# Kernel optimization log

Hardware: AMD Instinct MI355X
Metric: run time of the kernel (lower is better)

The kernel has to match this reference:

```python
import jax, jax.numpy as jnp
import numpy as np

NF, EF, H, G, T, LAYERS = 133, 14, 300, 200, 12, 3
B, N_PER, PAIRS = 4096, 32, 32
N, E = B * N_PER, B * PAIRS * 2
R1, R2 = 550, 378  # readout dims per config defaults


def setup_inputs() -> dict:
    key = jax.random.key(0)
    ks = jax.random.split(key, 16)
    rng = np.random.default_rng(0)
    # edges within each graph, laid out as reverse pairs: 2i = (u->w), 2i+1 = (w->u)
    u = rng.integers(0, N_PER, size=(B, PAIRS))
    w = (u + 1 + rng.integers(0, N_PER - 1, size=(B, PAIRS))) % N_PER  # w != u
    offs = (np.arange(B) * N_PER)[:, None]
    u, w = u + offs, w + offs
    src = np.stack([u, w], axis=-1).reshape(-1).astype(np.int64)
    dst = np.stack([w, u], axis=-1).reshape(-1).astype(np.int64)
    node_graph = np.repeat(np.arange(B), N_PER).astype(np.int64)

    def lin(k, fin, fout):
        s = (2.0 / (fin + fout)) ** 0.5  # xavier_normal, gain=1
        return jax.random.normal(k, (fin, fout), jnp.float32) * s

    return {
        "v": jax.random.normal(ks[0], (N, NF + 1), jnp.float32),
        "e": jax.random.normal(ks[1], (E, EF + 1), jnp.float32),
        "globals_": jax.random.normal(ks[2], (B, G), jnp.float32),
        "Wi": lin(ks[3], NF + EF, H), "bi": jnp.zeros((H,), jnp.float32),
        "Wm": lin(ks[4], H, H), "bm": jnp.zeros((H,), jnp.float32),
        "Wa": lin(ks[5], NF + H, H), "ba": jnp.zeros((H,), jnp.float32),
        "Wr1": lin(ks[6], G + H, R1), "br1": jnp.zeros((R1,), jnp.float32),
        "Wr2": lin(ks[7], R1, R2), "br2": jnp.zeros((R2,), jnp.float32),
        "Wr3": lin(ks[8], R2, T), "br3": jnp.zeros((T,), jnp.float32),
        "src": jnp.asarray(src), "dst": jnp.asarray(dst),
        "node_graph": jnp.asarray(node_graph),
    }


def reference(v, e, globals_, Wi, bi, Wm, bm, Wa, ba,
              Wr1, br1, Wr2, br2, Wr3, br3, src, dst, node_graph):
    n = v.shape[0]
    b = globals_.shape[0]
    vv = v[:, :NF]          # strip trailing 'r' column
    ee = e[:, :EF]
    # edge init: h_0 = relu(W_i [src_v ; e])
    h0 = jax.nn.relu(jnp.concatenate([vv[src], ee], axis=1) @ Wi + bi)  # [E,H]
    rev = jnp.arange(h0.shape[0]) ^ 1  # reverse-pair edge layout
    h = h0
    for _ in range(LAYERS):
        # non-backtracking line-graph sum: incoming-to-src minus reverse edge
        acc = jax.ops.segment_sum(h, dst, num_segments=n)   # [N,H]
        m_e = acc[src] - h[rev]                             # [E,H]
        h = jax.nn.relu(h0 + m_e @ Wm + bm)                 # dropout p=0
    # reverse-graph copy_e sum => aggregate edges by ORIGINAL src node
    m_v = jax.ops.segment_sum(h, src, num_segments=n)       # [N,H]
    h_v = jax.nn.relu(jnp.concatenate([vv, m_v], axis=1) @ Wa + ba)
    # mean readout per graph
    cnt = jax.ops.segment_sum(jnp.ones((n,), v.dtype), node_graph, num_segments=b)
    out = jax.ops.segment_sum(h_v, node_graph, num_segments=b) / cnt[:, None]
    out = jax.nn.relu(jnp.concatenate([out, globals_], axis=1) @ Wr1 + br1)
    out = jax.nn.relu(out @ Wr2 + br2)
    return out @ Wr3 + br3
```

## Files before the change

### kernel.cpp

```cpp
#include <hip/hip_runtime.h>

typedef __bf16 bf16x8 __attribute__((ext_vector_type(8)));
typedef float f32x4 __attribute__((ext_vector_type(4)));
typedef unsigned short u16;
typedef unsigned int u32;
typedef unsigned long long u64;

#define NF_ 133
#define EF_ 14
#define HD 300
#define KH 320
#define K0 160
#define K2 448
#define NT 19

__device__ __forceinline__ u16 f2bf(float f) {
    union { float f; u32 u; } v; v.f = f;
    u32 r = v.u + 0x7fffu + ((v.u >> 16) & 1u);
    return (u16)(r >> 16);
}

__global__ void prep_w(const float* __restrict__ W, u16* __restrict__ Wt,
                       int K, int N, int KP, int NP) {
    int idx = blockIdx.x * 256 + threadIdx.x;
    if (idx >= NP * KP) return;
    int n = idx / KP, k = idx - n * KP;
    float val = (k < K && n < N) ? W[k * N + n] : 0.f;
    Wt[idx] = f2bf(val);
}

__global__ void prep_glob(const float* __restrict__ glob, u16* __restrict__ Ar1) {
    int idx = blockIdx.x * 256 + threadIdx.x;
    if (idx >= 4096 * 212) return;
    int g = idx / 212, c = 300 + (idx - g * 212);
    float val = (c < 500) ? glob[g * 200 + (c - 300)] : 0.f;
    Ar1[g * 512 + c] = f2bf(val);
}

__global__ __launch_bounds__(512, 1) void gnn_mega(
    const float* __restrict__ vf, const float* __restrict__ ef,
    const int* __restrict__ src, const int* __restrict__ dst,
    const u16* __restrict__ WiT, const u16* __restrict__ WmT, const u16* __restrict__ WaT,
    const float* __restrict__ bi, const float* __restrict__ bm, const float* __restrict__ ba,
    u16* __restrict__ Ar1)
{
    __shared__ u16 sm[64 * KH];
    __shared__ u16 shT[8 * 2560];
    __shared__ u16 sAe[8 * 512];
    __shared__ u16 sSo[8 * 256];
    __shared__ int s_src[64], s_dst[64];

    const int g = blockIdx.x;
    const int tid = threadIdx.x;
    const int wave = tid >> 6;
    const int lane = tid & 63;
    const int lm = lane & 15;
    const int q = lane >> 4;

    if (tid < 64) {
        s_src[tid] = src[g * 64 + tid] - g * 32;
        s_dst[tid] = dst[g * 64 + tid] - g * 32;
    }
    __syncthreads();

    for (int i = tid; i < 10240; i += 512) ((u32*)shT)[i] = 0u;
    if (tid < 512) ((u32*)sm)[9728 + tid] = 0u;

    for (int idx = tid; idx < 4096; idx += 512) {
        int e = idx >> 6, k = idx & 63;
        u16 v = (s_dst[k] == s_src[e] && k != (e ^ 1)) ? (u16)0x3F80 : (u16)0;
        sAe[((k >> 3) << 9) + (e << 3) + (k & 7)] = v;
    }
    for (int idx = tid; idx < 2048; idx += 512) {
        int n = idx >> 6, k = idx & 63;
        sSo[((k >> 3) << 8) + (n << 3) + (k & 7)] = (s_src[k] == n) ? (u16)0x3F80 : (u16)0;
    }
    for (int idx = tid; idx < 64 * K0; idx += 512) {
        int ed = idx / K0, c = idx - ed * K0;
        float val = 0.f;
        if (c < NF_) val = vf[(size_t)(g * 32 + s_src[ed]) * (NF_ + 1) + c];
        else if (c < NF_ + EF_) val = ef[(size_t)(g * 64 + ed) * (EF_ + 1) + (c - NF_)];
        sm[((c >> 3) << 9) + (ed << 3) + (c & 7)] = f2bf(val);
    }
    __syncthreads();

    f32x4 h0r[3][4];
    float bmv[3];
    {
        f32x4 acc[3][4];
        #pragma unroll
        for (int t = 0; t < 3; ++t)
            #pragma unroll
            for (int mt = 0; mt < 4; ++mt) acc[t][mt] = (f32x4){0.f, 0.f, 0.f, 0.f};
        #pragma unroll
        for (int ks = 0; ks < 5; ++ks) {
            bf16x8 af[4];
            #pragma unroll
            for (int mt = 0; mt < 4; ++mt)
                af[mt] = *(const bf16x8*)&sm[((ks * 4 + q) << 9) + ((mt * 16 + lm) << 3)];
            #pragma unroll
            for (int t = 0; t < 3; ++t) {
                int j = 8 * t + wave;
                if (j < NT) {
                    bf16x8 bfr = *(const bf16x8*)&WiT[(j * 16 + lm) * K0 + ks * 32 + q * 8];
                    #pragma unroll
                    for (int mt = 0; mt < 4; ++mt)
                        acc[t][mt] = __builtin_amdgcn_mfma_f32_16x16x32_bf16(af[mt], bfr, acc[t][mt], 0, 0, 0);
                }
            }
        }
        #pragma unroll
        for (int t = 0; t < 3; ++t) {
            int j = 8 * t + wave;
            int n = j * 16 + lm;
            bool ok = (j < NT) && (n < HD);
            float bv = ok ? bi[n] : 0.f;
            bmv[t] = ok ? bm[n] : 0.f;
            #pragma unroll
            for (int mt = 0; mt < 4; ++mt) {
                u64 w = 0;
                #pragma unroll
                for (int r = 0; r < 4; ++r) {
                    float hv = acc[t][mt][r] + bv;
                    hv = hv > 0.f ? hv : 0.f;
                    h0r[t][mt][r] = hv;
                    w |= ((u64)f2bf(hv)) << (16 * r);
                }
                if (ok) *(u64*)&shT[(mt * 2 + (q >> 1)) * 2560 + n * 8 + (q & 1) * 4] = w;
            }
        }
    }

    for (int layer = 0; layer < 3; ++layer) {
        __syncthreads();
        {
            bf16x8 ae[2][4];
            #pragma unroll
            for (int ks = 0; ks < 2; ++ks)
                #pragma unroll
                for (int mt = 0; mt < 4; ++mt)
                    ae[ks][mt] = *(const bf16x8*)&sAe[((ks * 4 + q) << 9) + ((mt * 16 + lm) << 3)];
            #pragma unroll
            for (int t = 0; t < 3; ++t) {
                int j = 8 * t + wave;
                if (j < NT) {
                    int col = j * 16 + lm;
                    f32x4 mac[4];
                    #pragma unroll
                    for (int mt = 0; mt < 4; ++mt) mac[mt] = (f32x4){0.f, 0.f, 0.f, 0.f};
                    #pragma unroll
                    for (int ks = 0; ks < 2; ++ks) {
                        bf16x8 bfr = *(const bf16x8*)&shT[(ks * 4 + q) * 2560 + col * 8];
                        #pragma unroll
                        for (int mt = 0; mt < 4; ++mt)
                            mac[mt] = __builtin_amdgcn_mfma_f32_16x16x32_bf16(ae[ks][mt], bfr, mac[mt], 0, 0, 0);
                    }
                    int base = ((col >> 3) << 9) + (col & 7);
                    #pragma unroll
                    for (int mt = 0; mt < 4; ++mt)
                        #pragma unroll
                        for (int r = 0; r < 4; ++r)
                            sm[base + ((mt * 16 + q * 4 + r) << 3)] = f2bf(mac[mt][r]);
                }
            }
        }
        __syncthreads();
        {
            f32x4 acc[3][4];
            #pragma unroll
            for (int t = 0; t < 3; ++t)
                #pragma unroll
                for (int mt = 0; mt < 4; ++mt) acc[t][mt] = (f32x4){0.f, 0.f, 0.f, 0.f};
            #pragma unroll
            for (int ks = 0; ks < 10; ++ks) {
                bf16x8 af[4];
                #pragma unroll
                for (int mt = 0; mt < 4; ++mt)
                    af[mt] = *(const bf16x8*)&sm[((ks * 4 + q) << 9) + ((mt * 16 + lm) << 3)];
                #pragma unroll
                for (int t = 0; t < 3; ++t) {
                    int j = 8 * t + wave;
                    if (j < NT) {
                        bf16x8 bfr = *(const bf16x8*)&WmT[(j * 16 + lm) * KH + ks * 32 + q * 8];
                        #pragma unroll
                        for (int mt = 0; mt < 4; ++mt)
                            acc[t][mt] = __builtin_amdgcn_mfma_f32_16x16x32_bf16(af[mt], bfr, acc[t][mt], 0, 0, 0);
                    }
                }
            }
            #pragma unroll
            for (int t = 0; t < 3; ++t) {
                int j = 8 * t + wave;
                int n = j * 16 + lm;
                bool ok = (j < NT) && (n < HD);
                #pragma unroll
                for (int mt = 0; mt < 4; ++mt) {
                    u64 w = 0;
                    #pragma unroll
                    for (int r = 0; r < 4; ++r) {
                        float hv = h0r[t][mt][r] + acc[t][mt][r] + bmv[t];
                        hv = hv > 0.f ? hv : 0.f;
                        w |= ((u64)f2bf(hv)) << (16 * r);
                    }
                    if (ok) *(u64*)&shT[(mt * 2 + (q >> 1)) * 2560 + n * 8 + (q & 1) * 4] = w;
                }
            }
        }
    }
    __syncthreads();

    for (int idx = tid; idx < 32 * K2; idx += 512) {
        int n = idx / K2, c = idx - n * K2;
        float val = (c < NF_) ? vf[(size_t)(g * 32 + n) * (NF_ + 1) + c] : 0.f;
        sm[((c >> 3) << 8) + (n << 3) + (c & 7)] = f2bf(val);
    }
    __syncthreads();

    #pragma unroll
    for (int t = 0; t < 3; ++t) {
        int j = 8 * t + wave;
        if (j < NT) {
            int hc = j * 16 + lm;
            f32x4 vacc[2];
            #pragma unroll
            for (int mt = 0; mt < 2; ++mt) vacc[mt] = (f32x4){0.f, 0.f, 0.f, 0.f};
            #pragma unroll
            for (int ks = 0; ks < 2; ++ks) {
                bf16x8 bfr = *(const bf16x8*)&shT[(ks * 4 + q) * 2560 + hc * 8];
                #pragma unroll
                for (int mt = 0; mt < 2; ++mt) {
                    bf16x8 af = *(const bf16x8*)&sSo[((ks * 4 + q) << 8) + ((mt * 16 + lm) << 3)];
                    vacc[mt] = __builtin_amdgcn_mfma_f32_16x16x32_bf16(af, bfr, vacc[mt], 0, 0, 0);
                }
            }
            if (hc < HD) {
                int cc = NF_ + hc;
                int base = ((cc >> 3) << 8) + (cc & 7);
                #pragma unroll
                for (int mt = 0; mt < 2; ++mt)
                    #pragma unroll
                    for (int r = 0; r < 4; ++r)
                        sm[base + ((mt * 16 + q * 4 + r) << 3)] = f2bf(vacc[mt][r]);
            }
        }
    }
    __syncthreads();

    {
        f32x4 acc2[3][2];
        #pragma unroll
        for (int t = 0; t < 3; ++t)
            #pragma unroll
            for (int mt = 0; mt < 2; ++mt) acc2[t][mt] = (f32x4){0.f, 0.f, 0.f, 0.f};
        #pragma unroll
        for (int ks = 0; ks < 14; ++ks) {
            bf16x8 af[2];
            #pragma unroll
            for (int mt = 0; mt < 2; ++mt)
                af[mt] = *(const bf16x8*)&sm[((ks * 4 + q) << 8) + ((mt * 16 + lm) << 3)];
            #pragma unroll
            for (int t = 0; t < 3; ++t) {
                int j = 8 * t + wave;
                if (j < NT) {
                    bf16x8 bfr = *(const bf16x8*)&WaT[(j * 16 + lm) * K2 + ks * 32 + q * 8];
                    #pragma unroll
                    for (int mt = 0; mt < 2; ++mt)
                        acc2[t][mt] = __builtin_amdgcn_mfma_f32_16x16x32_bf16(af[mt], bfr, acc2[t][mt], 0, 0, 0);
                }
            }
        }
        #pragma unroll
        for (int t = 0; t < 3; ++t) {
            int j = 8 * t + wave;
            int n = j * 16 + lm;
            bool ok = (j < NT) && (n < HD);
            float bav = ok ? ba[n] : 0.f;
            float s = 0.f;
            #pragma unroll
            for (int mt = 0; mt < 2; ++mt)
                #pragma unroll
                for (int r = 0; r < 4; ++r) {
                    float hv = acc2[t][mt][r] + bav;
                    s += (hv > 0.f ? hv : 0.f);
                }
            s += __shfl_xor(s, 16);
            s += __shfl_xor(s, 32);
            if (ok && q == 0) Ar1[g * 512 + n] = f2bf(s * 0.03125f);
        }
    }
}

template<int RELU, int OUTBF16>
__global__ __launch_bounds__(256, 4) void gemm_ro(
    const u16* __restrict__ A, const u16* __restrict__ Bt, const float* __restrict__ bias,
    const int KP, const int Nreal, const int outPitch, void* __restrict__ outp, const int nsteps)
{
    const int tid = threadIdx.x;
    const int wv = tid >> 6, lane = tid & 63, lm = lane & 15, q = lane >> 4;
    const int row0 = blockIdx.x * 64;
    const int col = blockIdx.y * 64 + wv * 16 + lm;
    f32x4 acc[4];
    #pragma unroll
    for (int mt = 0; mt < 4; ++mt) acc[mt] = (f32x4){0.f, 0.f, 0.f, 0.f};
    const u16* bp = Bt + col * KP + q * 8;
    const u16* ap = A + (row0 + lm) * KP + q * 8;
    for (int ks = 0; ks < nsteps; ++ks) {
        bf16x8 bfr = *(const bf16x8*)(bp + ks * 32);
        #pragma unroll
        for (int mt = 0; mt < 4; ++mt) {
            bf16x8 afr = *(const bf16x8*)(ap + mt * 16 * KP + ks * 32);
            acc[mt] = __builtin_amdgcn_mfma_f32_16x16x32_bf16(afr, bfr, acc[mt], 0, 0, 0);
        }
    }
    const float bv = (col < Nreal) ? bias[col] : 0.f;
    #pragma unroll
    for (int mt = 0; mt < 4; ++mt) {
        #pragma unroll
        for (int r = 0; r < 4; ++r) {
            int row = row0 + mt * 16 + q * 4 + r;
            float val = acc[mt][r] + bv;
            if (RELU) val = val > 0.f ? val : 0.f;
            if (OUTBF16) {
                ((u16*)outp)[row * outPitch + col] = (col < Nreal) ? f2bf(val) : (u16)0;
            } else {
                if (col < Nreal) ((float*)outp)[row * outPitch + col] = val;
            }
        }
    }
}

extern "C" void kernel_launch(void* const* d_in, const int* in_sizes, int n_in,
                              void* d_out, int out_size, void* d_ws, size_t ws_size,
                              hipStream_t stream) {
    (void)in_sizes; (void)n_in; (void)out_size; (void)ws_size;
    const float* v   = (const float*)d_in[0];
    const float* e   = (const float*)d_in[1];
    const float* glb = (const float*)d_in[2];
    const float* Wi  = (const float*)d_in[3];
    const float* bi  = (const float*)d_in[4];
    const float* Wm  = (const float*)d_in[5];
    const float* bm  = (const float*)d_in[6];
    const float* Wa  = (const float*)d_in[7];
    const float* ba  = (const float*)d_in[8];
    const float* Wr1 = (const float*)d_in[9];
    const float* br1 = (const float*)d_in[10];
    const float* Wr2 = (const float*)d_in[11];
    const float* br2 = (const float*)d_in[12];
    const float* Wr3 = (const float*)d_in[13];
    const float* br3 = (const float*)d_in[14];
    const int* src = (const int*)d_in[15];
    const int* dst = (const int*)d_in[16];

    char* ws = (char*)d_ws;
    u16* WiT  = (u16*)(ws + 0);
    u16* WmT  = (u16*)(ws + 97280);
    u16* WaT  = (u16*)(ws + 291840);
    u16* Wr1T = (u16*)(ws + 564224);
    u16* Wr2T = (u16*)(ws + 1154048);
    u16* Wr3T = (u16*)(ws + 1596416);
    u16* Ar1  = (u16*)(ws + 1645568);
    u16* Ar2  = (u16*)(ws + 5839872);
    u16* Ar3  = (u16*)(ws + 10558464);

    prep_w<<<190,  256, 0, stream>>>(Wi,  WiT,  147, 300, 160, 304);
    prep_w<<<380,  256, 0, stream>>>(Wm,  WmT,  300, 300, 320, 304);
    prep_w<<<532,  256, 0, stream>>>(Wa,  WaT,  433, 300, 448, 304);
    prep_w<<<1152, 256, 0, stream>>>(Wr1, Wr1T, 500, 550, 512, 576);
    prep_w<<<864,  256, 0, stream>>>(Wr2, Wr2T, 550, 378, 576, 384);
    prep_w<<<96,   256, 0, stream>>>(Wr3, Wr3T, 378, 12,  384, 64);
    prep_glob<<<3392, 256, 0, stream>>>(glb, Ar1);

    gnn_mega<<<4096, 512, 0, stream>>>(v, e, src, dst, WiT, WmT, WaT, bi, bm, ba, Ar1);

    gemm_ro<1, 1><<<dim3(64, 9), 256, 0, stream>>>(Ar1, Wr1T, br1, 512, 550, 576, Ar2, 16);
    gemm_ro<1, 1><<<dim3(64, 6), 256, 0, stream>>>(Ar2, Wr2T, br2, 576, 378, 384, Ar3, 18);
    gemm_ro<0, 0><<<dim3(64, 1), 256, 0, stream>>>(Ar3, Wr3T, br3, 384, 12, 12, d_out, 12);
}
```

Baseline: 935.7 us.

## Build adjacency fragments from bitmasks in registers and pack h0 as bf16

```diff
diff --git a/kernel.cpp b/kernel.cpp
--- a/kernel.cpp
+++ b/kernel.cpp
@@ -13,19 +13,26 @@
 #define K0 160
 #define K2 448
 #define NT 19
+#define SHP 2432
 
 __device__ __forceinline__ u16 f2bf(float f) {
     union { float f; u32 u; } v; v.f = f;
     u32 r = v.u + 0x7fffu + ((v.u >> 16) & 1u);
     return (u16)(r >> 16);
 }
+__device__ __forceinline__ float bf2f(u16 h) {
+    union { u32 u; float f; } v; v.u = ((u32)h) << 16;
+    return v.f;
+}
 
 __global__ void prep_w(const float* __restrict__ W, u16* __restrict__ Wt,
-                       int K, int N, int KP, int NP) {
+                       int K, int N, int KP, int NP, int gap) {
     int idx = blockIdx.x * 256 + threadIdx.x;
     if (idx >= NP * KP) return;
     int n = idx / KP, k = idx - n * KP;
-    float val = (k < K && n < N) ? W[k * N + n] : 0.f;
+    int kk = k;
+    if (gap) kk = (k < 133) ? k : ((k >= 136 && k < 436) ? k - 3 : -1);
+    float val = (kk >= 0 && kk < K && n < N) ? W[kk * N + n] : 0.f;
     Wt[idx] = f2bf(val);
 }
 
@@ -37,7 +44,7 @@
     Ar1[g * 512 + c] = f2bf(val);
 }
 
-__global__ __launch_bounds__(512, 1) void gnn_mega(
+__global__ __launch_bounds__(512, 4) void gnn_mega(
     const float* __restrict__ vf, const float* __restrict__ ef,
     const int* __restrict__ src, const int* __restrict__ dst,
     const u16* __restrict__ WiT, const u16* __restrict__ WmT, const u16* __restrict__ WaT,
@@ -45,10 +52,11 @@
     u16* __restrict__ Ar1)
 {
     __shared__ u16 sm[64 * KH];
-    __shared__ u16 shT[8 * 2560];
-    __shared__ u16 sAe[8 * 512];
-    __shared__ u16 sSo[8 * 256];
-    __shared__ int s_src[64], s_dst[64];
+    __shared__ u16 shT[8 * SHP];
+    __shared__ u64 s_amask[32];
+    __shared__ u64 s_smask[32];
+    __shared__ int s_src[64];
+    __shared__ unsigned char s_src8[64];
 
     const int g = blockIdx.x;
     const int tid = threadIdx.x;
@@ -58,23 +66,21 @@
     const int q = lane >> 4;
 
     if (tid < 64) {
-        s_src[tid] = src[g * 64 + tid] - g * 32;
-        s_dst[tid] = dst[g * 64 + tid] - g * 32;
-    }
+        int sv = src[g * 64 + tid] - g * 32;
+        int dv = dst[g * 64 + tid] - g * 32;
+        s_src[tid] = sv;
+        s_src8[tid] = (unsigned char)sv;
+        #pragma unroll 1
+        for (int n = 0; n < 32; ++n) {
+            u64 bmA = __ballot(dv == n);
+            u64 bmS = __ballot(sv == n);
+            if (tid == 0) { s_amask[n] = bmA; s_smask[n] = bmS; }
+        }
+    }
+    for (int i = tid; i < 9728; i += 512) ((u32*)shT)[i] = 0u;
+    if (tid < 512) ((u32*)sm)[9728 + tid] = 0u;
     __syncthreads();
 
-    for (int i = tid; i < 10240; i += 512) ((u32*)shT)[i] = 0u;
-    if (tid < 512) ((u32*)sm)[9728 + tid] = 0u;
-
-    for (int idx = tid; idx < 4096; idx += 512) {
-        int e = idx >> 6, k = idx & 63;
-        u16 v = (s_dst[k] == s_src[e] && k != (e ^ 1)) ? (u16)0x3F80 : (u16)0;
-        sAe[((k >> 3) << 9) + (e << 3) + (k & 7)] = v;
-    }
-    for (int idx = tid; idx < 2048; idx += 512) {
-        int n = idx >> 6, k = idx & 63;
-        sSo[((k >> 3) << 8) + (n << 3) + (k & 7)] = (s_src[k] == n) ? (u16)0x3F80 : (u16)0;
-    }
     for (int idx = tid; idx < 64 * K0; idx += 512) {
         int ed = idx / K0, c = idx - ed * K0;
         float val = 0.f;
@@ -84,7 +90,7 @@
     }
     __syncthreads();
 
-    f32x4 h0r[3][4];
+    u64 h0p[3][4];
     float bmv[3];
     {
         f32x4 acc[3][4];
@@ -123,10 +129,10 @@
                 for (int r = 0; r < 4; ++r) {
                     float hv = acc[t][mt][r] + bv;
                     hv = hv > 0.f ? hv : 0.f;
-                    h0r[t][mt][r] = hv;
                     w |= ((u64)f2bf(hv)) << (16 * r);
                 }
-                if (ok) *(u64*)&shT[(mt * 2 + (q >> 1)) * 2560 + n * 8 + (q & 1) * 4] = w;
+                h0p[t][mt] = w;
+                if (ok) *(u64*)&shT[(mt * 2 + (q >> 1)) * SHP + n * 8 + (q & 1) * 4] = w;
             }
         }
     }
@@ -134,33 +140,49 @@
     for (int layer = 0; layer < 3; ++layer) {
         __syncthreads();
         {
-            bf16x8 ae[2][4];
-            #pragma unroll
-            for (int ks = 0; ks < 2; ++ks)
-                #pragma unroll
-                for (int mt = 0; mt < 4; ++mt)
-                    ae[ks][mt] = *(const bf16x8*)&sAe[((ks * 4 + q) << 9) + ((mt * 16 + lm) << 3)];
+            u64 am[4];
+            #pragma unroll
+            for (int mt = 0; mt < 4; ++mt) {
+                int e = mt * 16 + lm;
+                am[mt] = s_amask[s_src8[e]] & ~(1ull << (e ^ 1));
+            }
+            bf16x8 bfrag[2][4];
+            #pragma unroll
+            for (int ks = 0; ks < 2; ++ks) {
+                int kb = ks * 32 + q * 8;
+                #pragma unroll
+                for (int mt = 0; mt < 4; ++mt) {
+                    union { u32 w[4]; bf16x8 v; } fb;
+                    #pragma unroll
+                    for (int jj = 0; jj < 4; ++jj) {
+                        u32 lo = (u32)((am[mt] >> (kb + 2 * jj)) & 1ull) * 0x3F80u;
+                        u32 hi = (u32)((am[mt] >> (kb + 2 * jj + 1)) & 1ull) * 0x3F80u;
+                        fb.w[jj] = lo | (hi << 16);
+                    }
+                    bfrag[ks][mt] = fb.v;
+                }
+            }
             #pragma unroll
             for (int t = 0; t < 3; ++t) {
                 int j = 8 * t + wave;
                 if (j < NT) {
-                    int col = j * 16 + lm;
                     f32x4 mac[4];
                     #pragma unroll
                     for (int mt = 0; mt < 4; ++mt) mac[mt] = (f32x4){0.f, 0.f, 0.f, 0.f};
                     #pragma unroll
                     for (int ks = 0; ks < 2; ++ks) {
-                        bf16x8 bfr = *(const bf16x8*)&shT[(ks * 4 + q) * 2560 + col * 8];
+                        bf16x8 af = *(const bf16x8*)&shT[(ks * 4 + q) * SHP + (j * 16 + lm) * 8];
                         #pragma unroll
                         for (int mt = 0; mt < 4; ++mt)
-                            mac[mt] = __builtin_amdgcn_mfma_f32_16x16x32_bf16(ae[ks][mt], bfr, mac[mt], 0, 0, 0);
+                            mac[mt] = __builtin_amdgcn_mfma_f32_16x16x32_bf16(af, bfrag[ks][mt], mac[mt], 0, 0, 0);
                     }
-                    int base = ((col >> 3) << 9) + (col & 7);
-                    #pragma unroll
-                    for (int mt = 0; mt < 4; ++mt)
+                    #pragma unroll
+                    for (int mt = 0; mt < 4; ++mt) {
+                        u64 w = 0;
                         #pragma unroll
-                        for (int r = 0; r < 4; ++r)
-                            sm[base + ((mt * 16 + q * 4 + r) << 3)] = f2bf(mac[mt][r]);
+                        for (int r = 0; r < 4; ++r) w |= ((u64)f2bf(mac[mt][r])) << (16 * r);
+                        *(u64*)&sm[(j * 2 + (q >> 1)) * 512 + (mt * 16 + lm) * 8 + (q & 1) * 4] = w;
+                    }
                 }
             }
         }
@@ -198,11 +220,12 @@
                     u64 w = 0;
                     #pragma unroll
                     for (int r = 0; r < 4; ++r) {
-                        float hv = h0r[t][mt][r] + acc[t][mt][r] + bmv[t];
+                        float h0v = bf2f((u16)(h0p[t][mt] >> (16 * r)));
+                        float hv = h0v + acc[t][mt][r] + bmv[t];
                         hv = hv > 0.f ? hv : 0.f;
                         w |= ((u64)f2bf(hv)) << (16 * r);
                     }
-                    if (ok) *(u64*)&shT[(mt * 2 + (q >> 1)) * 2560 + n * 8 + (q & 1) * 4] = w;
+                    if (ok) *(u64*)&shT[(mt * 2 + (q >> 1)) * SHP + n * 8 + (q & 1) * 4] = w;
                 }
             }
         }
@@ -216,31 +239,45 @@
     }
     __syncthreads();
 
-    #pragma unroll
-    for (int t = 0; t < 3; ++t) {
-        int j = 8 * t + wave;
-        if (j < NT) {
-            int hc = j * 16 + lm;
-            f32x4 vacc[2];
-            #pragma unroll
-            for (int mt = 0; mt < 2; ++mt) vacc[mt] = (f32x4){0.f, 0.f, 0.f, 0.f};
-            #pragma unroll
-            for (int ks = 0; ks < 2; ++ks) {
-                bf16x8 bfr = *(const bf16x8*)&shT[(ks * 4 + q) * 2560 + hc * 8];
+    {
+        bf16x8 sfrag[2][2];
+        #pragma unroll
+        for (int ks = 0; ks < 2; ++ks) {
+            int kb = ks * 32 + q * 8;
+            #pragma unroll
+            for (int mt = 0; mt < 2; ++mt) {
+                u64 msk = s_smask[mt * 16 + lm];
+                union { u32 w[4]; bf16x8 v; } fb;
+                #pragma unroll
+                for (int jj = 0; jj < 4; ++jj) {
+                    u32 lo = (u32)((msk >> (kb + 2 * jj)) & 1ull) * 0x3F80u;
+                    u32 hi = (u32)((msk >> (kb + 2 * jj + 1)) & 1ull) * 0x3F80u;
+                    fb.w[jj] = lo | (hi << 16);
+                }
+                sfrag[ks][mt] = fb.v;
+            }
+        }
+        #pragma unroll
+        for (int t = 0; t < 3; ++t) {
+            int j = 8 * t + wave;
+            if (j < NT) {
+                f32x4 vacc[2];
+                #pragma unroll
+                for (int mt = 0; mt < 2; ++mt) vacc[mt] = (f32x4){0.f, 0.f, 0.f, 0.f};
+                #pragma unroll
+                for (int ks = 0; ks < 2; ++ks) {
+                    bf16x8 af = *(const bf16x8*)&shT[(ks * 4 + q) * SHP + (j * 16 + lm) * 8];
+                    #pragma unroll
+                    for (int mt = 0; mt < 2; ++mt)
+                        vacc[mt] = __builtin_amdgcn_mfma_f32_16x16x32_bf16(af, sfrag[ks][mt], vacc[mt], 0, 0, 0);
+                }
                 #pragma unroll
                 for (int mt = 0; mt < 2; ++mt) {
-                    bf16x8 af = *(const bf16x8*)&sSo[((ks * 4 + q) << 8) + ((mt * 16 + lm) << 3)];
-                    vacc[mt] = __builtin_amdgcn_mfma_f32_16x16x32_bf16(af, bfr, vacc[mt], 0, 0, 0);
-                }
-            }
-            if (hc < HD) {
-                int cc = NF_ + hc;
-                int base = ((cc >> 3) << 8) + (cc & 7);
-                #pragma unroll
-                for (int mt = 0; mt < 2; ++mt)
-                    #pragma unroll
-                    for (int r = 0; r < 4; ++r)
-                        sm[base + ((mt * 16 + q * 4 + r) << 3)] = f2bf(vacc[mt][r]);
+                    u64 w = 0;
+                    #pragma unroll
+                    for (int r = 0; r < 4; ++r) w |= ((u64)f2bf(vacc[mt][r])) << (16 * r);
+                    *(u64*)&sm[(17 + j * 2 + (q >> 1)) * 256 + (mt * 16 + lm) * 8 + (q & 1) * 4] = w;
+                }
             }
         }
     }
@@ -362,12 +399,12 @@
     u16* Ar2  = (u16*)(ws + 5839872);
     u16* Ar3  = (u16*)(ws + 10558464);
 
-    prep_w<<<190,  256, 0, stream>>>(Wi,  WiT,  147, 300, 160, 304);
-    prep_w<<<380,  256, 0, stream>>>(Wm,  WmT,  300, 300, 320, 304);
-    prep_w<<<532,  256, 0, stream>>>(Wa,  WaT,  433, 300, 448, 304);
-    prep_w<<<1152, 256, 0, stream>>>(Wr1, Wr1T, 500, 550, 512, 576);
-    prep_w<<<864,  256, 0, stream>>>(Wr2, Wr2T, 550, 378, 576, 384);
-    prep_w<<<96,   256, 0, stream>>>(Wr3, Wr3T, 378, 12,  384, 64);
+    prep_w<<<190,  256, 0, stream>>>(Wi,  WiT,  147, 300, 160, 304, 0);
+    prep_w<<<380,  256, 0, stream>>>(Wm,  WmT,  300, 300, 320, 304, 0);
+    prep_w<<<532,  256, 0, stream>>>(Wa,  WaT,  433, 300, 448, 304, 1);
+    prep_w<<<1152, 256, 0, stream>>>(Wr1, Wr1T, 500, 550, 512, 576, 0);
+    prep_w<<<864,  256, 0, stream>>>(Wr2, Wr2T, 550, 378, 576, 384, 0);
+    prep_w<<<96,   256, 0, stream>>>(Wr3, Wr3T, 378, 12,  384, 64,  0);
     prep_glob<<<3392, 256, 0, stream>>>(glb, Ar1);
 
     gnn_mega<<<4096, 512, 0, stream>>>(v, e, src, dst, WiT, WmT, WaT, bi, bm, ba, Ar1);
```

New measurement: 1.426 ms. 52.4% more time.
